# Optimization experiments

Hardware: AMD Instinct MI355X
Metric: run time of the kernel (lower is better)

The kernel has to match this reference:

```python
import jax, jax.numpy as jnp
import numpy as np

B, S, IN = 1, 50000, 128
N = B * S
E = 800000
HID, HEADS, OUT = 64, 2, 64
NEG_SLOPE = 0.2
BN_EPS = 1e-5


def setup_inputs() -> dict:
    key = jax.random.key(0)
    ks = jax.random.split(key, 12)
    s = 0.1
    return {
        "data": jax.random.normal(ks[0], (B, S, IN), jnp.float32),
        "edge_index": jax.random.randint(ks[1], (2, E), 0, N, dtype=jnp.int64),
        "W0": jax.random.normal(ks[2], (IN, HEADS * HID), jnp.float32) * s,
        "att_src0": jax.random.normal(ks[3], (HEADS, HID), jnp.float32) * s,
        "att_dst0": jax.random.normal(ks[4], (HEADS, HID), jnp.float32) * s,
        "bias0": jnp.zeros((HEADS * HID,), jnp.float32),
        "gamma0": jnp.ones((HEADS * HID,), jnp.float32),
        "beta0": jnp.zeros((HEADS * HID,), jnp.float32),
        "W1": jax.random.normal(ks[5], (HEADS * HID, OUT), jnp.float32) * s,
        "att_src1": jax.random.normal(ks[6], (1, OUT), jnp.float32) * s,
        "att_dst1": jax.random.normal(ks[7], (1, OUT), jnp.float32) * s,
        "bias1": jnp.zeros((OUT,), jnp.float32),
    }


def gat_conv(x, edge_index, W, att_src, att_dst, bias, heads, ch, concat):
    n = x.shape[0]
    loop = jnp.arange(n, dtype=edge_index.dtype)
    src = jnp.concatenate([edge_index[0], loop])  # PyG adds self-loops by default
    dst = jnp.concatenate([edge_index[1], loop])
    h = (x @ W).reshape(n, heads, ch)  # [N,H,C]
    a_src = (h * att_src).sum(-1)  # [N,H]
    a_dst = (h * att_dst).sum(-1)  # [N,H]
    e = jax.nn.leaky_relu(a_src[src] + a_dst[dst], NEG_SLOPE)  # [Etot,H]
    m = jax.ops.segment_max(e, dst, num_segments=n)  # segment softmax over dst
    ex = jnp.exp(e - m[dst])
    denom = jax.ops.segment_sum(ex, dst, num_segments=n)
    alpha = ex / (denom[dst] + 1e-16)  # [Etot,H]
    out = jax.ops.segment_sum(h[src] * alpha[:, :, None], dst, num_segments=n)  # [N,H,C]
    out = out.reshape(n, heads * ch) if concat else out.mean(axis=1)
    return out + bias


def reference(data, edge_index, W0, att_src0, att_dst0, bias0, gamma0, beta0,
              W1, att_src1, att_dst1, bias1):
    x = data.reshape(N, IN)
    x = gat_conv(x, edge_index, W0, att_src0, att_dst0, bias0, HEADS, HID, True)
    mu = x.mean(axis=0)
    var = x.var(axis=0)
    x = (x - mu) * jax.lax.rsqrt(var + BN_EPS) * gamma0 + beta0  # BatchNorm1d (batch stats)
    x = jax.nn.elu(x)
    x = gat_conv(x, edge_index, W1, att_src1, att_dst1, bias1, 1, OUT, False)
    return x.reshape(B, S, OUT)
```

## Files before the change

kernel.cpp:

```cpp
#include <hip/hip_runtime.h>
#include <hip/hip_fp16.h>
#include <math.h>

#define N_NODES 50000
#define E_EDGES 800000
#define NEG_SLOPE 0.2f
#define BN_EPS 1e-5f

#define BK_SHIFT 9
#define NBK 98
#define L1_BLOCKS 256
#define L1_CHUNK (E_EDGES / L1_BLOCKS)
#define CNT_N (NBK * L1_BLOCKS)
#define SCG_BLOCKS ((CNT_N + 1023) / 1024)
#define STAGE_MAX 9216

typedef __attribute__((ext_vector_type(8))) _Float16 half8;
typedef __attribute__((ext_vector_type(4))) float f32x4;

__device__ __forceinline__ float lrelu(float v) { return v > 0.f ? v : NEG_SLOPE * v; }

__global__ void k_zero(float* __restrict__ bn_sum, float* __restrict__ bn_sumsq) {
  int t = threadIdx.x;
  if (t < 128) { bn_sum[t] = 0.f; bn_sumsq[t] = 0.f; }
}

__global__ __launch_bounds__(256) void k_cvtx(const float* __restrict__ x,
                                              _Float16* __restrict__ xh) {
  int i = blockIdx.x * 256 + threadIdx.x;
  const float4* p = (const float4*)x + (size_t)i * 2;
  float4 a = p[0], b = p[1];
  half8 o = {(_Float16)a.x, (_Float16)a.y, (_Float16)a.z, (_Float16)a.w,
             (_Float16)b.x, (_Float16)b.y, (_Float16)b.z, (_Float16)b.w};
  *((half8*)xh + i) = o;
}

__global__ void k_cvtW(const float* __restrict__ W0, const float* __restrict__ W1,
                       _Float16* __restrict__ W0t, _Float16* __restrict__ W1t) {
  int t = threadIdx.x;
  for (int idx = t; idx < 128 * 128; idx += 256) {
    int k = idx >> 7, c = idx & 127;
    W0t[c * 128 + k] = (_Float16)W0[idx];
  }
  for (int idx = t; idx < 128 * 64; idx += 256) {
    int k = idx >> 6, c = idx & 63;
    W1t[c * 128 + k] = (_Float16)W1[idx];
  }
}

__global__ __launch_bounds__(256) void k_cvty(const float* __restrict__ x,
                                              const float* __restrict__ scale,
                                              const float* __restrict__ shift,
                                              _Float16* __restrict__ yh) {
  int i = blockIdx.x * 256 + threadIdx.x;
  int c = (i * 8) & 127;
  float4 s0 = *(const float4*)&scale[c], s1 = *(const float4*)&scale[c + 4];
  float4 f0 = *(const float4*)&shift[c], f1 = *(const float4*)&shift[c + 4];
  const float4* p = (const float4*)x + (size_t)i * 2;
  float4 a = p[0], b = p[1];
  float v[8];
  v[0] = a.x * s0.x + f0.x; v[1] = a.y * s0.y + f0.y;
  v[2] = a.z * s0.z + f0.z; v[3] = a.w * s0.w + f0.w;
  v[4] = b.x * s1.x + f1.x; v[5] = b.y * s1.y + f1.y;
  v[6] = b.z * s1.z + f1.z; v[7] = b.w * s1.w + f1.w;
  half8 o;
#pragma unroll
  for (int j = 0; j < 8; j++) {
    float e = v[j] > 0.f ? v[j] : __expf(v[j]) - 1.f;
    o[j] = (_Float16)e;
  }
  *((half8*)yh + i) = o;
}

__global__ __launch_bounds__(256) void k_l1hist(const int* __restrict__ dst,
                                                int* __restrict__ cnt) {
  __shared__ int lcnt[NBK];
  int t = threadIdx.x;
  if (t < NBK) lcnt[t] = 0;
  __syncthreads();
  int beg = blockIdx.x * L1_CHUNK, end = beg + L1_CHUNK;
  for (int e = beg + t; e < end; e += 256)
    atomicAdd(&lcnt[((unsigned int)dst[e]) >> BK_SHIFT], 1);
  __syncthreads();
  for (int b = t; b < NBK; b += 256) cnt[b * L1_BLOCKS + blockIdx.x] = lcnt[b];
}

__global__ __launch_bounds__(256) void k_scan1g(const int* __restrict__ cnt,
                                                int* __restrict__ tmp,
                                                int* __restrict__ bsums) {
  __shared__ int ts[256];
  int t = threadIdx.x;
  int base = blockIdx.x * 1024 + t * 4;
  int c0 = (base + 0 < CNT_N) ? cnt[base + 0] : 0;
  int c1 = (base + 1 < CNT_N) ? cnt[base + 1] : 0;
  int c2 = (base + 2 < CNT_N) ? cnt[base + 2] : 0;
  int c3 = (base + 3 < CNT_N) ? cnt[base + 3] : 0;
  int s = c0 + c1 + c2 + c3;
  ts[t] = s;
  __syncthreads();
  for (int off = 1; off < 256; off <<= 1) {
    int v = (t >= off) ? ts[t - off] : 0;
    __syncthreads();
    ts[t] += v;
    __syncthreads();
  }
  int excl = ts[t] - s;
  if (t == 255) bsums[blockIdx.x] = ts[255];
  if (base + 0 < CNT_N) tmp[base + 0] = excl;
  if (base + 1 < CNT_N) tmp[base + 1] = excl + c0;
  if (base + 2 < CNT_N) tmp[base + 2] = excl + c0 + c1;
  if (base + 3 < CNT_N) tmp[base + 3] = excl + c0 + c1 + c2;
}

__global__ void k_scan2g(int* __restrict__ bsums) {
  int t = threadIdx.x;
  int orig = (t < SCG_BLOCKS) ? bsums[t] : 0;
  int v = orig;
#pragma unroll
  for (int off = 1; off < 64; off <<= 1) {
    int u = __shfl_up(v, off);
    if (t >= off) v += u;
  }
  if (t < SCG_BLOCKS) bsums[t] = v - orig;
}

__global__ __launch_bounds__(256) void k_l1scatter(const int* __restrict__ src,
                                                   const int* __restrict__ dst,
                                                   const int* __restrict__ tmp,
                                                   const int* __restrict__ bsums,
                                                   unsigned int* __restrict__ binned) {
  __shared__ int cur[NBK];
  int t = threadIdx.x;
  for (int b = t; b < NBK; b += 256) {
    int idx = b * L1_BLOCKS + blockIdx.x;
    cur[b] = tmp[idx] + bsums[idx >> 10];
  }
  __syncthreads();
  int beg = blockIdx.x * L1_CHUNK, end = beg + L1_CHUNK;
  for (int e = beg + t; e < end; e += 256) {
    unsigned int d = (unsigned int)dst[e];
    int b = d >> BK_SHIFT;
    int p = atomicAdd(&cur[b], 1);
    binned[p] = ((unsigned int)src[e] << 16) | d;
  }
}

__global__ void k_bbase(const int* __restrict__ tmp, const int* __restrict__ bsums,
                        int* __restrict__ bucket_base) {
  int b = threadIdx.x;
  if (b < NBK) {
    int idx = b * L1_BLOCKS;
    bucket_base[b] = tmp[idx] + bsums[idx >> 10];
  }
  if (b == NBK) bucket_base[NBK] = E_EDGES;
}

__global__ __launch_bounds__(256) void k_scatter3(const int* __restrict__ bucket_base,
                                                  const unsigned int* __restrict__ binned,
                                                  int* __restrict__ row_ptr,
                                                  int* __restrict__ csr_src) {
  __shared__ int cnt[512];
  __shared__ int staging[STAGE_MAX];
  __shared__ int ts[256];
  int t = threadIdx.x;
  int b = blockIdx.x;
  int lo = b << BK_SHIFT;
  int hi = lo + 512; if (hi > N_NODES) hi = N_NODES;
  int nloc = hi - lo;
  int base = bucket_base[b];
  int end = bucket_base[b + 1];
  cnt[t] = 0; cnt[t + 256] = 0;
  __syncthreads();
  for (int i = base + t; i < end; i += 256)
    atomicAdd(&cnt[(binned[i] & 0xFFFFu) - lo], 1);
  __syncthreads();
  int c0 = cnt[2 * t], c1 = cnt[2 * t + 1];
  int pair = c0 + c1;
  ts[t] = pair;
  __syncthreads();
  for (int off = 1; off < 256; off <<= 1) {
    int v = (t >= off) ? ts[t - off] : 0;
    __syncthreads();
    ts[t] += v;
    __syncthreads();
  }
  int exclp = ts[t] - pair;
  cnt[2 * t] = exclp;
  cnt[2 * t + 1] = exclp + c0;
  if (2 * t < nloc) row_ptr[lo + 2 * t] = base + exclp;
  if (2 * t + 1 < nloc) row_ptr[lo + 2 * t + 1] = base + exclp + c0;
  if (b == NBK - 1 && t == 0) row_ptr[N_NODES] = E_EDGES;
  __syncthreads();
  for (int i = base + t; i < end; i += 256) {
    unsigned int v = binned[i];
    int d = (int)(v & 0xFFFFu) - lo;
    int p = atomicAdd(&cnt[d], 1);
    int s = (int)(v >> 16);
    if (p < STAGE_MAX) staging[p] = s;
    else csr_src[base + p] = s;
  }
  __syncthreads();
  int tot = end - base;
  int lim = tot < STAGE_MAX ? tot : STAGE_MAX;
  for (int k = t; k < lim; k += 256) csr_src[base + k] = staging[k];
}

__global__ __launch_bounds__(256) void k_gemm0m(
    const _Float16* __restrict__ xh, const _Float16* __restrict__ Wt,
    const float* __restrict__ att_s, const float* __restrict__ att_d,
    _Float16* __restrict__ h, float* __restrict__ a_src, float* __restrict__ a_dst) {
  int lane = threadIdx.x & 63;
  int wv = threadIdx.x >> 6;
  int row0 = blockIdx.x * 64 + wv * 16;
  int m = lane & 15, kg = lane >> 4;
  int arow = row0 + m;
  int arowc = arow < N_NODES ? arow : N_NODES - 1;
  f32x4 acc[8];
#pragma unroll
  for (int ct = 0; ct < 8; ct++) acc[ct] = (f32x4){0.f, 0.f, 0.f, 0.f};
#pragma unroll
  for (int kc = 0; kc < 4; kc++) {
    half8 af = *(const half8*)&xh[(size_t)arowc * 128 + kc * 32 + kg * 8];
#pragma unroll
    for (int ct = 0; ct < 8; ct++) {
      half8 bf = *(const half8*)&Wt[(ct * 16 + m) * 128 + kc * 32 + kg * 8];
      acc[ct] = __builtin_amdgcn_mfma_f32_16x16x32_f16(af, bf, acc[ct], 0, 0, 0);
    }
  }
  float as[8], ad[8];
#pragma unroll
  for (int ct = 0; ct < 8; ct++) { as[ct] = att_s[ct * 16 + m]; ad[ct] = att_d[ct * 16 + m]; }
#pragma unroll
  for (int r = 0; r < 4; r++) {
    int row = row0 + kg * 4 + r;
    bool ok = row < N_NODES;
    float ps0 = 0.f, pd0 = 0.f, ps1 = 0.f, pd1 = 0.f;
#pragma unroll
    for (int ct = 0; ct < 4; ct++) { ps0 += acc[ct][r] * as[ct]; pd0 += acc[ct][r] * ad[ct]; }
#pragma unroll
    for (int ct = 4; ct < 8; ct++) { ps1 += acc[ct][r] * as[ct]; pd1 += acc[ct][r] * ad[ct]; }
#pragma unroll
    for (int msk = 1; msk <= 8; msk <<= 1) {
      ps0 += __shfl_xor(ps0, msk); pd0 += __shfl_xor(pd0, msk);
      ps1 += __shfl_xor(ps1, msk); pd1 += __shfl_xor(pd1, msk);
    }
    if (ok) {
#pragma unroll
      for (int ct = 0; ct < 8; ct++)
        h[(size_t)row * 128 + ct * 16 + m] = (_Float16)acc[ct][r];
      if (m == 0) {
        a_src[row * 2 + 0] = ps0; a_dst[row * 2 + 0] = pd0;
        a_src[row * 2 + 1] = ps1; a_dst[row * 2 + 1] = pd1;
      }
    }
  }
}

__global__ __launch_bounds__(256) void k_gemm1m(
    const _Float16* __restrict__ yh, const _Float16* __restrict__ Wt,
    const float* __restrict__ att_s, const float* __restrict__ att_d,
    _Float16* __restrict__ h, float* __restrict__ a_src, float* __restrict__ a_dst) {
  int lane = threadIdx.x & 63;
  int wv = threadIdx.x >> 6;
  int row0 = blockIdx.x * 64 + wv * 16;
  int m = lane & 15, kg = lane >> 4;
  int arow = row0 + m;
  int arowc = arow < N_NODES ? arow : N_NODES - 1;
  f32x4 acc[4];
#pragma unroll
  for (int ct = 0; ct < 4; ct++) acc[ct] = (f32x4){0.f, 0.f, 0.f, 0.f};
#pragma unroll
  for (int kc = 0; kc < 4; kc++) {
    half8 af = *(const half8*)&yh[(size_t)arowc * 128 + kc * 32 + kg * 8];
#pragma unroll
    for (int ct = 0; ct < 4; ct++) {
      half8 bf = *(const half8*)&Wt[(ct * 16 + m) * 128 + kc * 32 + kg * 8];
      acc[ct] = __builtin_amdgcn_mfma_f32_16x16x32_f16(af, bf, acc[ct], 0, 0, 0);
    }
  }
  float as[4], ad[4];
#pragma unroll
  for (int ct = 0; ct < 4; ct++) { as[ct] = att_s[ct * 16 + m]; ad[ct] = att_d[ct * 16 + m]; }
#pragma unroll
  for (int r = 0; r < 4; r++) {
    int row = row0 + kg * 4 + r;
    bool ok = row < N_NODES;
    float ps = 0.f, pd = 0.f;
#pragma unroll
    for (int ct = 0; ct < 4; ct++) { ps += acc[ct][r] * as[ct]; pd += acc[ct][r] * ad[ct]; }
#pragma unroll
    for (int msk = 1; msk <= 8; msk <<= 1) {
      ps += __shfl_xor(ps, msk); pd += __shfl_xor(pd, msk);
    }
    if (ok) {
#pragma unroll
      for (int ct = 0; ct < 4; ct++)
        h[(size_t)row * 64 + ct * 16 + m] = (_Float16)acc[ct][r];
      if (m == 0) { a_src[row] = ps; a_dst[row] = pd; }
    }
  }
}

__global__ __launch_bounds__(256) void k_agg0(
    const int* __restrict__ row_ptr, const int* __restrict__ csr_src,
    const __half* __restrict__ h, const float* __restrict__ a_src,
    const float* __restrict__ a_dst, const float* __restrict__ bias,
    float* __restrict__ out) {
  int node = (blockIdx.x * blockDim.x + threadIdx.x) >> 6;
  if (node >= N_NODES) return;
  int l = threadIdx.x & 63;
  int head = l >> 5;
  int c = l * 2;
  float ad = a_dst[node * 2 + head];
  float m = lrelu(a_src[node * 2 + head] + ad);
  float d = 1.f;
  float2 hv = __half22float2(*(const __half2*)&h[(size_t)node * 128 + c]);
  float acc0 = hv.x, acc1 = hv.y;
  int beg = row_ptr[node], end = row_ptr[node + 1];
  int i = beg;
  for (; i + 8 <= end; i += 8) {
    int s0 = csr_src[i], s1 = csr_src[i + 1], s2 = csr_src[i + 2], s3 = csr_src[i + 3];
    int s4 = csr_src[i + 4], s5 = csr_src[i + 5], s6 = csr_src[i + 6], s7 = csr_src[i + 7];
    float e0 = lrelu(a_src[s0 * 2 + head] + ad), e1 = lrelu(a_src[s1 * 2 + head] + ad);
    float e2 = lrelu(a_src[s2 * 2 + head] + ad), e3 = lrelu(a_src[s3 * 2 + head] + ad);
    float e4 = lrelu(a_src[s4 * 2 + head] + ad), e5 = lrelu(a_src[s5 * 2 + head] + ad);
    float e6 = lrelu(a_src[s6 * 2 + head] + ad), e7 = lrelu(a_src[s7 * 2 + head] + ad);
    __half2 p0 = *(const __half2*)&h[(size_t)s0 * 128 + c];
    __half2 p1 = *(const __half2*)&h[(size_t)s1 * 128 + c];
    __half2 p2 = *(const __half2*)&h[(size_t)s2 * 128 + c];
    __half2 p3 = *(const __half2*)&h[(size_t)s3 * 128 + c];
    __half2 p4 = *(const __half2*)&h[(size_t)s4 * 128 + c];
    __half2 p5 = *(const __half2*)&h[(size_t)s5 * 128 + c];
    __half2 p6 = *(const __half2*)&h[(size_t)s6 * 128 + c];
    __half2 p7 = *(const __half2*)&h[(size_t)s7 * 128 + c];
    float nm = fmaxf(m, fmaxf(fmaxf(fmaxf(e0, e1), fmaxf(e2, e3)),
                              fmaxf(fmaxf(e4, e5), fmaxf(e6, e7))));
    float sc = __expf(m - nm);
    float w0 = __expf(e0 - nm), w1 = __expf(e1 - nm), w2 = __expf(e2 - nm), w3 = __expf(e3 - nm);
    float w4 = __expf(e4 - nm), w5 = __expf(e5 - nm), w6 = __expf(e6 - nm), w7 = __expf(e7 - nm);
    d = d * sc + ((w0 + w1) + (w2 + w3)) + ((w4 + w5) + (w6 + w7));
    float2 f0 = __half22float2(p0), f1 = __half22float2(p1);
    float2 f2 = __half22float2(p2), f3 = __half22float2(p3);
    float2 f4 = __half22float2(p4), f5 = __half22float2(p5);
    float2 f6 = __half22float2(p6), f7 = __half22float2(p7);
    acc0 = acc0 * sc + (w0 * f0.x + w1 * f1.x + w2 * f2.x + w3 * f3.x) +
           (w4 * f4.x + w5 * f5.x + w6 * f6.x + w7 * f7.x);
    acc1 = acc1 * sc + (w0 * f0.y + w1 * f1.y + w2 * f2.y + w3 * f3.y) +
           (w4 * f4.y + w5 * f5.y + w6 * f6.y + w7 * f7.y);
    m = nm;
  }
  for (; i + 4 <= end; i += 4) {
    int s0 = csr_src[i], s1 = csr_src[i + 1], s2 = csr_src[i + 2], s3 = csr_src[i + 3];
    float e0 = lrelu(a_src[s0 * 2 + head] + ad), e1 = lrelu(a_src[s1 * 2 + head] + ad);
    float e2 = lrelu(a_src[s2 * 2 + head] + ad), e3 = lrelu(a_src[s3 * 2 + head] + ad);
    __half2 p0 = *(const __half2*)&h[(size_t)s0 * 128 + c];
    __half2 p1 = *(const __half2*)&h[(size_t)s1 * 128 + c];
    __half2 p2 = *(const __half2*)&h[(size_t)s2 * 128 + c];
    __half2 p3 = *(const __half2*)&h[(size_t)s3 * 128 + c];
    float nm = fmaxf(fmaxf(m, e0), fmaxf(fmaxf(e1, e2), e3));
    float sc = __expf(m - nm);
    float w0 = __expf(e0 - nm), w1 = __expf(e1 - nm), w2 = __expf(e2 - nm), w3 = __expf(e3 - nm);
    d = d * sc + (w0 + w1) + (w2 + w3);
    float2 f0 = __half22float2(p0), f1 = __half22float2(p1);
    float2 f2 = __half22float2(p2), f3 = __half22float2(p3);
    acc0 = acc0 * sc + w0 * f0.x + w1 * f1.x + w2 * f2.x + w3 * f3.x;
    acc1 = acc1 * sc + w0 * f0.y + w1 * f1.y + w2 * f2.y + w3 * f3.y;
    m = nm;
  }
  for (; i < end; i++) {
    int s = csr_src[i];
    float ee = lrelu(a_src[s * 2 + head] + ad);
    __half2 pp = *(const __half2*)&h[(size_t)s * 128 + c];
    float nm = fmaxf(m, ee);
    float sc = __expf(m - nm);
    float w = __expf(ee - nm);
    float2 ff = __half22float2(pp);
    d = d * sc + w;
    acc0 = acc0 * sc + w * ff.x;
    acc1 = acc1 * sc + w * ff.y;
    m = nm;
  }
  float inv = 1.f / d;
  float2 o;
  o.x = acc0 * inv + bias[c];
  o.y = acc1 * inv + bias[c + 1];
  *(float2*)&out[(size_t)node * 128 + c] = o;
}

__global__ __launch_bounds__(256) void k_bnstats(const float* __restrict__ x,
                                                 float* __restrict__ bn_sum,
                                                 float* __restrict__ bn_sumsq) {
  int f = threadIdx.x & 127;
  int half = threadIdx.x >> 7;
  float s = 0.f, s2 = 0.f;
  for (int r = blockIdx.x * 2 + half; r < N_NODES; r += gridDim.x * 2) {
    float v = x[(size_t)r * 128 + f];
    s += v;
    s2 += v * v;
  }
  __shared__ float ls[256], ls2[256];
  ls[threadIdx.x] = s;
  ls2[threadIdx.x] = s2;
  __syncthreads();
  if (half == 0) {
    atomicAdd(&bn_sum[f], s + ls[f + 128]);
    atomicAdd(&bn_sumsq[f], s2 + ls2[f + 128]);
  }
}

__global__ void k_bnfinal(const float* __restrict__ sum, const float* __restrict__ sumsq,
                          const float* __restrict__ gamma, const float* __restrict__ beta,
                          float* __restrict__ scale, float* __restrict__ shift) {
  int f = threadIdx.x;
  float mu = sum[f] / (float)N_NODES;
  float var = sumsq[f] / (float)N_NODES - mu * mu;
  float sc = gamma[f] * rsqrtf(var + BN_EPS);
  scale[f] = sc;
  shift[f] = beta[f] - mu * sc;
}

__global__ __launch_bounds__(256) void k_agg1(
    const int* __restrict__ row_ptr, const int* __restrict__ csr_src,
    const __half* __restrict__ h, const float* __restrict__ a_src,
    const float* __restrict__ a_dst, const float* __restrict__ bias,
    float* __restrict__ out) {
  int node = (blockIdx.x * blockDim.x + threadIdx.x) >> 6;
  if (node >= N_NODES) return;
  int l = threadIdx.x & 63;
  float ad = a_dst[node];
  float m = lrelu(a_src[node] + ad);
  float d = 1.f;
  float acc = __half2float(h[(size_t)node * 64 + l]);
  int beg = row_ptr[node], end = row_ptr[node + 1];
  int i = beg;
  for (; i + 8 <= end; i += 8) {
    int s0 = csr_src[i], s1 = csr_src[i + 1], s2 = csr_src[i + 2], s3 = csr_src[i + 3];
    int s4 = csr_src[i + 4], s5 = csr_src[i + 5], s6 = csr_src[i + 6], s7 = csr_src[i + 7];
    float e0 = lrelu(a_src[s0] + ad), e1 = lrelu(a_src[s1] + ad);
    float e2 = lrelu(a_src[s2] + ad), e3 = lrelu(a_src[s3] + ad);
    float e4 = lrelu(a_src[s4] + ad), e5 = lrelu(a_src[s5] + ad);
    float e6 = lrelu(a_src[s6] + ad), e7 = lrelu(a_src[s7] + ad);
    __half p0 = h[(size_t)s0 * 64 + l], p1 = h[(size_t)s1 * 64 + l];
    __half p2 = h[(size_t)s2 * 64 + l], p3 = h[(size_t)s3 * 64 + l];
    __half p4 = h[(size_t)s4 * 64 + l], p5 = h[(size_t)s5 * 64 + l];
    __half p6 = h[(size_t)s6 * 64 + l], p7 = h[(size_t)s7 * 64 + l];
    float nm = fmaxf(m, fmaxf(fmaxf(fmaxf(e0, e1), fmaxf(e2, e3)),
                              fmaxf(fmaxf(e4, e5), fmaxf(e6, e7))));
    float sc = __expf(m - nm);
    float w0 = __expf(e0 - nm), w1 = __expf(e1 - nm), w2 = __expf(e2 - nm), w3 = __expf(e3 - nm);
    float w4 = __expf(e4 - nm), w5 = __expf(e5 - nm), w6 = __expf(e6 - nm), w7 = __expf(e7 - nm);
    d = d * sc + ((w0 + w1) + (w2 + w3)) + ((w4 + w5) + (w6 + w7));
    acc = acc * sc +
          (w0 * __half2float(p0) + w1 * __half2float(p1) + w2 * __half2float(p2) +
           w3 * __half2float(p3)) +
          (w4 * __half2float(p4) + w5 * __half2float(p5) + w6 * __half2float(p6) +
           w7 * __half2float(p7));
    m = nm;
  }
  for (; i + 4 <= end; i += 4) {
    int s0 = csr_src[i], s1 = csr_src[i + 1], s2 = csr_src[i + 2], s3 = csr_src[i + 3];
    float e0 = lrelu(a_src[s0] + ad), e1 = lrelu(a_src[s1] + ad);
    float e2 = lrelu(a_src[s2] + ad), e3 = lrelu(a_src[s3] + ad);
    __half p0 = h[(size_t)s0 * 64 + l], p1 = h[(size_t)s1 * 64 + l];
    __half p2 = h[(size_t)s2 * 64 + l], p3 = h[(size_t)s3 * 64 + l];
    float nm = fmaxf(fmaxf(m, e0), fmaxf(fmaxf(e1, e2), e3));
    float sc = __expf(m - nm);
    float w0 = __expf(e0 - nm), w1 = __expf(e1 - nm), w2 = __expf(e2 - nm), w3 = __expf(e3 - nm);
    d = d * sc + (w0 + w1) + (w2 + w3);
    acc = acc * sc + w0 * __half2float(p0) + w1 * __half2float(p1) + w2 * __half2float(p2) +
          w3 * __half2float(p3);
    m = nm;
  }
  for (; i < end; i++) {
    int s = csr_src[i];
    float ee = lrelu(a_src[s] + ad);
    __half pp = h[(size_t)s * 64 + l];
    float nm = fmaxf(m, ee);
    float sc = __expf(m - nm);
    float w = __expf(ee - nm);
    d = d * sc + w;
    acc = acc * sc + w * __half2float(pp);
    m = nm;
  }
  out[(size_t)node * 64 + l] = acc / d + bias[l];
}

extern "C" void kernel_launch(void* const* d_in, const int* in_sizes, int n_in,
                              void* d_out, int out_size, void* d_ws, size_t ws_size,
                              hipStream_t stream) {
  const float* data = (const float*)d_in[0];
  const int* ei = (const int*)d_in[1];
  const float* W0 = (const float*)d_in[2];
  const float* att_src0 = (const float*)d_in[3];
  const float* att_dst0 = (const float*)d_in[4];
  const float* bias0 = (const float*)d_in[5];
  const float* gamma0 = (const float*)d_in[6];
  const float* beta0 = (const float*)d_in[7];
  const float* W1 = (const float*)d_in[8];
  const float* att_src1 = (const float*)d_in[9];
  const float* att_dst1 = (const float*)d_in[10];
  const float* bias1 = (const float*)d_in[11];
  float* out = (float*)d_out;

  char* ws = (char*)d_ws;
  size_t off = 0;
  auto alloc = [&](size_t bytes) -> void* {
    void* p = ws + off;
    off = (off + bytes + 255) & ~(size_t)255;
    return p;
  };
  int* cnt = (int*)alloc((size_t)CNT_N * 4);
  int* tmp = (int*)alloc((size_t)CNT_N * 4);
  int* bsums = (int*)alloc(32 * 4);
  int* bucket_base = (int*)alloc((NBK + 1) * 4);
  int* row_ptr = (int*)alloc((N_NODES + 1) * 4);
  unsigned int* binned = (unsigned int*)alloc((size_t)E_EDGES * 4);
  int* csr_src = (int*)alloc((size_t)E_EDGES * 4);
  _Float16* xh = (_Float16*)alloc((size_t)N_NODES * 128 * 2);
  _Float16* W0t = (_Float16*)alloc(128 * 128 * 2);
  _Float16* W1t = (_Float16*)alloc(64 * 128 * 2);
  _Float16* h0 = (_Float16*)alloc((size_t)N_NODES * 128 * 2);
  float* a_s0 = (float*)alloc((size_t)N_NODES * 2 * 4);
  float* a_d0 = (float*)alloc((size_t)N_NODES * 2 * 4);
  float* out0 = (float*)alloc((size_t)N_NODES * 128 * 4);
  _Float16* yh = (_Float16*)alloc((size_t)N_NODES * 128 * 2);
  float* bn_sum = (float*)alloc(128 * 4);
  float* bn_sumsq = (float*)alloc(128 * 4);
  float* bn_scale = (float*)alloc(128 * 4);
  float* bn_shift = (float*)alloc(128 * 4);
  _Float16* h1 = h0;
  float* a_s1 = a_s0;
  float* a_d1 = a_d0;

  const int* srcArr = ei;
  const int* dstArr = ei + E_EDGES;

  k_zero<<<1, 128, 0, stream>>>(bn_sum, bn_sumsq);
  k_cvtW<<<1, 256, 0, stream>>>(W0, W1, W0t, W1t);
  k_cvtx<<<3125, 256, 0, stream>>>(data, xh);
  k_l1hist<<<L1_BLOCKS, 256, 0, stream>>>(dstArr, cnt);
  k_scan1g<<<SCG_BLOCKS, 256, 0, stream>>>(cnt, tmp, bsums);
  k_scan2g<<<1, 64, 0, stream>>>(bsums);
  k_l1scatter<<<L1_BLOCKS, 256, 0, stream>>>(srcArr, dstArr, tmp, bsums, binned);
  k_bbase<<<1, 128, 0, stream>>>(tmp, bsums, bucket_base);
  k_scatter3<<<NBK, 256, 0, stream>>>(bucket_base, binned, row_ptr, csr_src);
  k_gemm0m<<<(N_NODES + 63) / 64, 256, 0, stream>>>(xh, W0t, att_src0, att_dst0, h0, a_s0, a_d0);
  k_agg0<<<(N_NODES + 3) / 4, 256, 0, stream>>>(row_ptr, csr_src, (const __half*)h0, a_s0, a_d0,
                                                bias0, out0);
  k_bnstats<<<1024, 256, 0, stream>>>(out0, bn_sum, bn_sumsq);
  k_bnfinal<<<1, 128, 0, stream>>>(bn_sum, bn_sumsq, gamma0, beta0, bn_scale, bn_shift);
  k_cvty<<<3125, 256, 0, stream>>>(out0, bn_scale, bn_shift, yh);
  k_gemm1m<<<(N_NODES + 63) / 64, 256, 0, stream>>>(yh, W1t, att_src1, att_dst1, h1, a_s1, a_d1);
  k_agg1<<<(N_NODES + 3) / 4, 256, 0, stream>>>(row_ptr, csr_src, (const __half*)h1, a_s1, a_d1,
                                                bias1, out);
}
```

Baseline: 307.5 us.

## Fuse input conversions into GEMMs and split aggregation into weight and accumulate passes

The fp32-to-fp16 conversion of the input and the BatchNorm+ELU conversion are folded into the GEMM A-operand loads, which removes two elementwise kernels and their fp16 intermediate buffers. Each GAT aggregation is split in two. A wave-parallel kernel computes the normalized softmax weights per edge and writes them to memory. A second kernel gathers features using those precomputed weights, with no online max/rescale in the inner loop. This adds an extra pass over the CSR and an edge-weight array to write and read back, in exchange for a simpler, more parallel accumulate loop.

```diff
diff --git a/kernel.cpp b/kernel.cpp
--- a/kernel.cpp
+++ b/kernel.cpp
@@ -25,16 +25,6 @@
   if (t < 128) { bn_sum[t] = 0.f; bn_sumsq[t] = 0.f; }
 }
 
-__global__ __launch_bounds__(256) void k_cvtx(const float* __restrict__ x,
-                                              _Float16* __restrict__ xh) {
-  int i = blockIdx.x * 256 + threadIdx.x;
-  const float4* p = (const float4*)x + (size_t)i * 2;
-  float4 a = p[0], b = p[1];
-  half8 o = {(_Float16)a.x, (_Float16)a.y, (_Float16)a.z, (_Float16)a.w,
-             (_Float16)b.x, (_Float16)b.y, (_Float16)b.z, (_Float16)b.w};
-  *((half8*)xh + i) = o;
-}
-
 __global__ void k_cvtW(const float* __restrict__ W0, const float* __restrict__ W1,
                        _Float16* __restrict__ W0t, _Float16* __restrict__ W1t) {
   int t = threadIdx.x;
@@ -46,30 +36,6 @@
     int k = idx >> 6, c = idx & 63;
     W1t[c * 128 + k] = (_Float16)W1[idx];
   }
-}
-
-__global__ __launch_bounds__(256) void k_cvty(const float* __restrict__ x,
-                                              const float* __restrict__ scale,
-                                              const float* __restrict__ shift,
-                                              _Float16* __restrict__ yh) {
-  int i = blockIdx.x * 256 + threadIdx.x;
-  int c = (i * 8) & 127;
-  float4 s0 = *(const float4*)&scale[c], s1 = *(const float4*)&scale[c + 4];
-  float4 f0 = *(const float4*)&shift[c], f1 = *(const float4*)&shift[c + 4];
-  const float4* p = (const float4*)x + (size_t)i * 2;
-  float4 a = p[0], b = p[1];
-  float v[8];
-  v[0] = a.x * s0.x + f0.x; v[1] = a.y * s0.y + f0.y;
-  v[2] = a.z * s0.z + f0.z; v[3] = a.w * s0.w + f0.w;
-  v[4] = b.x * s1.x + f1.x; v[5] = b.y * s1.y + f1.y;
-  v[6] = b.z * s1.z + f1.z; v[7] = b.w * s1.w + f1.w;
-  half8 o;
-#pragma unroll
-  for (int j = 0; j < 8; j++) {
-    float e = v[j] > 0.f ? v[j] : __expf(v[j]) - 1.f;
-    o[j] = (_Float16)e;
-  }
-  *((half8*)yh + i) = o;
 }
 
 __global__ __launch_bounds__(256) void k_l1hist(const int* __restrict__ dst,
@@ -206,7 +172,7 @@
 }
 
 __global__ __launch_bounds__(256) void k_gemm0m(
-    const _Float16* __restrict__ xh, const _Float16* __restrict__ Wt,
+    const float* __restrict__ x, const _Float16* __restrict__ Wt,
     const float* __restrict__ att_s, const float* __restrict__ att_d,
     _Float16* __restrict__ h, float* __restrict__ a_src, float* __restrict__ a_dst) {
   int lane = threadIdx.x & 63;
@@ -220,7 +186,11 @@
   for (int ct = 0; ct < 8; ct++) acc[ct] = (f32x4){0.f, 0.f, 0.f, 0.f};
 #pragma unroll
   for (int kc = 0; kc < 4; kc++) {
-    half8 af = *(const half8*)&xh[(size_t)arowc * 128 + kc * 32 + kg * 8];
+    const float* xp = &x[(size_t)arowc * 128 + kc * 32 + kg * 8];
+    float4 xa = *(const float4*)xp;
+    float4 xb = *(const float4*)(xp + 4);
+    half8 af = {(_Float16)xa.x, (_Float16)xa.y, (_Float16)xa.z, (_Float16)xa.w,
+                (_Float16)xb.x, (_Float16)xb.y, (_Float16)xb.z, (_Float16)xb.w};
 #pragma unroll
     for (int ct = 0; ct < 8; ct++) {
       half8 bf = *(const half8*)&Wt[(ct * 16 + m) * 128 + kc * 32 + kg * 8];
@@ -257,7 +227,8 @@
 }
 
 __global__ __launch_bounds__(256) void k_gemm1m(
-    const _Float16* __restrict__ yh, const _Float16* __restrict__ Wt,
+    const float* __restrict__ y, const float* __restrict__ scale,
+    const float* __restrict__ shift, const _Float16* __restrict__ Wt,
     const float* __restrict__ att_s, const float* __restrict__ att_d,
     _Float16* __restrict__ h, float* __restrict__ a_src, float* __restrict__ a_dst) {
   int lane = threadIdx.x & 63;
@@ -271,10 +242,26 @@
   for (int ct = 0; ct < 4; ct++) acc[ct] = (f32x4){0.f, 0.f, 0.f, 0.f};
 #pragma unroll
   for (int kc = 0; kc < 4; kc++) {
-    half8 af = *(const half8*)&yh[(size_t)arowc * 128 + kc * 32 + kg * 8];
+    int kb = kc * 32 + kg * 8;
+    const float* yp = &y[(size_t)arowc * 128 + kb];
+    float4 ya = *(const float4*)yp;
+    float4 yb = *(const float4*)(yp + 4);
+    float4 sa = *(const float4*)&scale[kb], sb = *(const float4*)&scale[kb + 4];
+    float4 fa = *(const float4*)&shift[kb], fb = *(const float4*)&shift[kb + 4];
+    float v[8];
+    v[0] = ya.x * sa.x + fa.x; v[1] = ya.y * sa.y + fa.y;
+    v[2] = ya.z * sa.z + fa.z; v[3] = ya.w * sa.w + fa.w;
+    v[4] = yb.x * sb.x + fb.x; v[5] = yb.y * sb.y + fb.y;
+    v[6] = yb.z * sb.z + fb.z; v[7] = yb.w * sb.w + fb.w;
+    half8 af;
+#pragma unroll
+    for (int j = 0; j < 8; j++) {
+      float e = v[j] > 0.f ? v[j] : __expf(v[j]) - 1.f;
+      af[j] = (_Float16)e;
+    }
 #pragma unroll
     for (int ct = 0; ct < 4; ct++) {
-      half8 bf = *(const half8*)&Wt[(ct * 16 + m) * 128 + kc * 32 + kg * 8];
+      half8 bf = *(const half8*)&Wt[(ct * 16 + m) * 128 + kb];
       acc[ct] = __builtin_amdgcn_mfma_f32_16x16x32_f16(af, bf, acc[ct], 0, 0, 0);
     }
   }
@@ -301,89 +288,93 @@
   }
 }
 
-__global__ __launch_bounds__(256) void k_agg0(
+__global__ __launch_bounds__(256) void k_wts0(
     const int* __restrict__ row_ptr, const int* __restrict__ csr_src,
-    const __half* __restrict__ h, const float* __restrict__ a_src,
-    const float* __restrict__ a_dst, const float* __restrict__ bias,
+    const float* __restrict__ a_src, const float* __restrict__ a_dst,
+    float2* __restrict__ wts, float2* __restrict__ selfw) {
+  int node = (blockIdx.x * blockDim.x + threadIdx.x) >> 6;
+  if (node >= N_NODES) return;
+  int l = threadIdx.x & 63;
+  float ad0 = a_dst[node * 2], ad1 = a_dst[node * 2 + 1];
+  float es0 = lrelu(a_src[node * 2] + ad0);
+  float es1 = lrelu(a_src[node * 2 + 1] + ad1);
+  int beg = row_ptr[node], end = row_ptr[node + 1];
+  const float NEGBIG = -3.0e38f;
+  float m0 = NEGBIG, s0 = 0.f, m1 = NEGBIG, s1 = 0.f;
+  for (int j = beg + l; j < end; j += 64) {
+    int s = csr_src[j];
+    float e0 = lrelu(a_src[s * 2] + ad0);
+    float e1 = lrelu(a_src[s * 2 + 1] + ad1);
+    float nm0 = fmaxf(m0, e0);
+    s0 = s0 * __expf(m0 - nm0) + __expf(e0 - nm0); m0 = nm0;
+    float nm1 = fmaxf(m1, e1);
+    s1 = s1 * __expf(m1 - nm1) + __expf(e1 - nm1); m1 = nm1;
+  }
+#pragma unroll
+  for (int msk = 1; msk < 64; msk <<= 1) {
+    float om0 = __shfl_xor(m0, msk), os0 = __shfl_xor(s0, msk);
+    float nm0 = fmaxf(m0, om0);
+    s0 = s0 * __expf(m0 - nm0) + os0 * __expf(om0 - nm0); m0 = nm0;
+    float om1 = __shfl_xor(m1, msk), os1 = __shfl_xor(s1, msk);
+    float nm1 = fmaxf(m1, om1);
+    s1 = s1 * __expf(m1 - nm1) + os1 * __expf(om1 - nm1); m1 = nm1;
+  }
+  float fm0 = fmaxf(m0, es0);
+  float d0 = s0 * __expf(m0 - fm0) + __expf(es0 - fm0);
+  float fm1 = fmaxf(m1, es1);
+  float d1 = s1 * __expf(m1 - fm1) + __expf(es1 - fm1);
+  float inv0 = 1.f / d0, inv1 = 1.f / d1;
+  for (int j = beg + l; j < end; j += 64) {
+    int s = csr_src[j];
+    float e0 = lrelu(a_src[s * 2] + ad0);
+    float e1 = lrelu(a_src[s * 2 + 1] + ad1);
+    wts[j] = make_float2(__expf(e0 - fm0) * inv0, __expf(e1 - fm1) * inv1);
+  }
+  if (l == 0) selfw[node] = make_float2(__expf(es0 - fm0) * inv0, __expf(es1 - fm1) * inv1);
+}
+
+__global__ __launch_bounds__(256) void k_acc0(
+    const int* __restrict__ row_ptr, const int* __restrict__ csr_src,
+    const __half* __restrict__ h, const float2* __restrict__ wts,
+    const float2* __restrict__ selfw, const float* __restrict__ bias,
     float* __restrict__ out) {
   int node = (blockIdx.x * blockDim.x + threadIdx.x) >> 6;
   if (node >= N_NODES) return;
   int l = threadIdx.x & 63;
   int head = l >> 5;
   int c = l * 2;
-  float ad = a_dst[node * 2 + head];
-  float m = lrelu(a_src[node * 2 + head] + ad);
-  float d = 1.f;
+  float2 sw = selfw[node];
+  float aself = head ? sw.y : sw.x;
   float2 hv = __half22float2(*(const __half2*)&h[(size_t)node * 128 + c]);
-  float acc0 = hv.x, acc1 = hv.y;
+  float acc0 = aself * hv.x, acc1 = aself * hv.y;
+  float bcc0 = 0.f, bcc1 = 0.f;
   int beg = row_ptr[node], end = row_ptr[node + 1];
-  int i = beg;
-  for (; i + 8 <= end; i += 8) {
-    int s0 = csr_src[i], s1 = csr_src[i + 1], s2 = csr_src[i + 2], s3 = csr_src[i + 3];
-    int s4 = csr_src[i + 4], s5 = csr_src[i + 5], s6 = csr_src[i + 6], s7 = csr_src[i + 7];
-    float e0 = lrelu(a_src[s0 * 2 + head] + ad), e1 = lrelu(a_src[s1 * 2 + head] + ad);
-    float e2 = lrelu(a_src[s2 * 2 + head] + ad), e3 = lrelu(a_src[s3 * 2 + head] + ad);
-    float e4 = lrelu(a_src[s4 * 2 + head] + ad), e5 = lrelu(a_src[s5 * 2 + head] + ad);
-    float e6 = lrelu(a_src[s6 * 2 + head] + ad), e7 = lrelu(a_src[s7 * 2 + head] + ad);
-    __half2 p0 = *(const __half2*)&h[(size_t)s0 * 128 + c];
-    __half2 p1 = *(const __half2*)&h[(size_t)s1 * 128 + c];
-    __half2 p2 = *(const __half2*)&h[(size_t)s2 * 128 + c];
-    __half2 p3 = *(const __half2*)&h[(size_t)s3 * 128 + c];
-    __half2 p4 = *(const __half2*)&h[(size_t)s4 * 128 + c];
-    __half2 p5 = *(const __half2*)&h[(size_t)s5 * 128 + c];
-    __half2 p6 = *(const __half2*)&h[(size_t)s6 * 128 + c];
-    __half2 p7 = *(const __half2*)&h[(size_t)s7 * 128 + c];
-    float nm = fmaxf(m, fmaxf(fmaxf(fmaxf(e0, e1), fmaxf(e2, e3)),
-                              fmaxf(fmaxf(e4, e5), fmaxf(e6, e7))));
-    float sc = __expf(m - nm);
-    float w0 = __expf(e0 - nm), w1 = __expf(e1 - nm), w2 = __expf(e2 - nm), w3 = __expf(e3 - nm);
-    float w4 = __expf(e4 - nm), w5 = __expf(e5 - nm), w6 = __expf(e6 - nm), w7 = __expf(e7 - nm);
-    d = d * sc + ((w0 + w1) + (w2 + w3)) + ((w4 + w5) + (w6 + w7));
-    float2 f0 = __half22float2(p0), f1 = __half22float2(p1);
-    float2 f2 = __half22float2(p2), f3 = __half22float2(p3);
-    float2 f4 = __half22float2(p4), f5 = __half22float2(p5);
-    float2 f6 = __half22float2(p6), f7 = __half22float2(p7);
-    acc0 = acc0 * sc + (w0 * f0.x + w1 * f1.x + w2 * f2.x + w3 * f3.x) +
-           (w4 * f4.x + w5 * f5.x + w6 * f6.x + w7 * f7.x);
-    acc1 = acc1 * sc + (w0 * f0.y + w1 * f1.y + w2 * f2.y + w3 * f3.y) +
-           (w4 * f4.y + w5 * f5.y + w6 * f6.y + w7 * f7.y);
-    m = nm;
-  }
-  for (; i + 4 <= end; i += 4) {
-    int s0 = csr_src[i], s1 = csr_src[i + 1], s2 = csr_src[i + 2], s3 = csr_src[i + 3];
-    float e0 = lrelu(a_src[s0 * 2 + head] + ad), e1 = lrelu(a_src[s1 * 2 + head] + ad);
-    float e2 = lrelu(a_src[s2 * 2 + head] + ad), e3 = lrelu(a_src[s3 * 2 + head] + ad);
-    __half2 p0 = *(const __half2*)&h[(size_t)s0 * 128 + c];
-    __half2 p1 = *(const __half2*)&h[(size_t)s1 * 128 + c];
-    __half2 p2 = *(const __half2*)&h[(size_t)s2 * 128 + c];
-    __half2 p3 = *(const __half2*)&h[(size_t)s3 * 128 + c];
-    float nm = fmaxf(fmaxf(m, e0), fmaxf(fmaxf(e1, e2), e3));
-    float sc = __expf(m - nm);
-    float w0 = __expf(e0 - nm), w1 = __expf(e1 - nm), w2 = __expf(e2 - nm), w3 = __expf(e3 - nm);
-    d = d * sc + (w0 + w1) + (w2 + w3);
-    float2 f0 = __half22float2(p0), f1 = __half22float2(p1);
-    float2 f2 = __half22float2(p2), f3 = __half22float2(p3);
-    acc0 = acc0 * sc + w0 * f0.x + w1 * f1.x + w2 * f2.x + w3 * f3.x;
-    acc1 = acc1 * sc + w0 * f0.y + w1 * f1.y + w2 * f2.y + w3 * f3.y;
-    m = nm;
-  }
-  for (; i < end; i++) {
-    int s = csr_src[i];
-    float ee = lrelu(a_src[s * 2 + head] + ad);
-    __half2 pp = *(const __half2*)&h[(size_t)s * 128 + c];
-    float nm = fmaxf(m, ee);
-    float sc = __expf(m - nm);
-    float w = __expf(ee - nm);
-    float2 ff = __half22float2(pp);
-    d = d * sc + w;
-    acc0 = acc0 * sc + w * ff.x;
-    acc1 = acc1 * sc + w * ff.y;
-    m = nm;
-  }
-  float inv = 1.f / d;
+  int j = beg;
+  for (; j + 4 <= end; j += 4) {
+    int s0 = csr_src[j], s1 = csr_src[j + 1], s2 = csr_src[j + 2], s3 = csr_src[j + 3];
+    float2 w0 = wts[j], w1 = wts[j + 1], w2 = wts[j + 2], w3 = wts[j + 3];
+    float a0 = head ? w0.y : w0.x, a1 = head ? w1.y : w1.x;
+    float a2 = head ? w2.y : w2.x, a3 = head ? w3.y : w3.x;
+    float2 f0 = __half22float2(*(const __half2*)&h[(size_t)s0 * 128 + c]);
+    float2 f1 = __half22float2(*(const __half2*)&h[(size_t)s1 * 128 + c]);
+    float2 f2 = __half22float2(*(const __half2*)&h[(size_t)s2 * 128 + c]);
+    float2 f3 = __half22float2(*(const __half2*)&h[(size_t)s3 * 128 + c]);
+    acc0 += a0 * f0.x + a2 * f2.x;
+    bcc0 += a1 * f1.x + a3 * f3.x;
+    acc1 += a0 * f0.y + a2 * f2.y;
+    bcc1 += a1 * f1.y + a3 * f3.y;
+  }
+  for (; j < end; j++) {
+    int s = csr_src[j];
+    float2 w = wts[j];
+    float a = head ? w.y : w.x;
+    float2 f = __half22float2(*(const __half2*)&h[(size_t)s * 128 + c]);
+    acc0 += a * f.x;
+    acc1 += a * f.y;
+  }
   float2 o;
-  o.x = acc0 * inv + bias[c];
-  o.y = acc1 * inv + bias[c + 1];
+  o.x = acc0 + bcc0 + bias[c];
+  o.y = acc1 + bcc1 + bias[c + 1];
   *(float2*)&out[(size_t)node * 128 + c] = o;
 }
 
@@ -419,70 +410,68 @@
   shift[f] = beta[f] - mu * sc;
 }
 
-__global__ __launch_bounds__(256) void k_agg1(
+__global__ __launch_bounds__(256) void k_wts1(
     const int* __restrict__ row_ptr, const int* __restrict__ csr_src,
-    const __half* __restrict__ h, const float* __restrict__ a_src,
-    const float* __restrict__ a_dst, const float* __restrict__ bias,
+    const float* __restrict__ a_src, const float* __restrict__ a_dst,
+    float* __restrict__ wts, float* __restrict__ selfw) {
+  int node = (blockIdx.x * blockDim.x + threadIdx.x) >> 6;
+  if (node >= N_NODES) return;
+  int l = threadIdx.x & 63;
+  float ad = a_dst[node];
+  float es = lrelu(a_src[node] + ad);
+  int beg = row_ptr[node], end = row_ptr[node + 1];
+  const float NEGBIG = -3.0e38f;
+  float m = NEGBIG, s = 0.f;
+  for (int j = beg + l; j < end; j += 64) {
+    int sn = csr_src[j];
+    float e = lrelu(a_src[sn] + ad);
+    float nm = fmaxf(m, e);
+    s = s * __expf(m - nm) + __expf(e - nm); m = nm;
+  }
+#pragma unroll
+  for (int msk = 1; msk < 64; msk <<= 1) {
+    float om = __shfl_xor(m, msk), os = __shfl_xor(s, msk);
+    float nm = fmaxf(m, om);
+    s = s * __expf(m - nm) + os * __expf(om - nm); m = nm;
+  }
+  float fm = fmaxf(m, es);
+  float d = s * __expf(m - fm) + __expf(es - fm);
+  float inv = 1.f / d;
+  for (int j = beg + l; j < end; j += 64) {
+    int sn = csr_src[j];
+    float e = lrelu(a_src[sn] + ad);
+    wts[j] = __expf(e - fm) * inv;
+  }
+  if (l == 0) selfw[node] = __expf(es - fm) * inv;
+}
+
+__global__ __launch_bounds__(256) void k_acc1(
+    const int* __restrict__ row_ptr, const int* __restrict__ csr_src,
+    const __half* __restrict__ h, const float* __restrict__ wts,
+    const float* __restrict__ selfw, const float* __restrict__ bias,
     float* __restrict__ out) {
   int node = (blockIdx.x * blockDim.x + threadIdx.x) >> 6;
   if (node >= N_NODES) return;
   int l = threadIdx.x & 63;
-  float ad = a_dst[node];
-  float m = lrelu(a_src[node] + ad);
-  float d = 1.f;
-  float acc = __half2float(h[(size_t)node * 64 + l]);
+  float acc = selfw[node] * __half2float(h[(size_t)node * 64 + l]);
+  float bcc = 0.f;
   int beg = row_ptr[node], end = row_ptr[node + 1];
-  int i = beg;
-  for (; i + 8 <= end; i += 8) {
-    int s0 = csr_src[i], s1 = csr_src[i + 1], s2 = csr_src[i + 2], s3 = csr_src[i + 3];
-    int s4 = csr_src[i + 4], s5 = csr_src[i + 5], s6 = csr_src[i + 6], s7 = csr_src[i + 7];
-    float e0 = lrelu(a_src[s0] + ad), e1 = lrelu(a_src[s1] + ad);
-    float e2 = lrelu(a_src[s2] + ad), e3 = lrelu(a_src[s3] + ad);
-    float e4 = lrelu(a_src[s4] + ad), e5 = lrelu(a_src[s5] + ad);
-    float e6 = lrelu(a_src[s6] + ad), e7 = lrelu(a_src[s7] + ad);
-    __half p0 = h[(size_t)s0 * 64 + l], p1 = h[(size_t)s1 * 64 + l];
-    __half p2 = h[(size_t)s2 * 64 + l], p3 = h[(size_t)s3 * 64 + l];
-    __half p4 = h[(size_t)s4 * 64 + l], p5 = h[(size_t)s5 * 64 + l];
-    __half p6 = h[(size_t)s6 * 64 + l], p7 = h[(size_t)s7 * 64 + l];
-    float nm = fmaxf(m, fmaxf(fmaxf(fmaxf(e0, e1), fmaxf(e2, e3)),
-                              fmaxf(fmaxf(e4, e5), fmaxf(e6, e7))));
-    float sc = __expf(m - nm);
-    float w0 = __expf(e0 - nm), w1 = __expf(e1 - nm), w2 = __expf(e2 - nm), w3 = __expf(e3 - nm);
-    float w4 = __expf(e4 - nm), w5 = __expf(e5 - nm), w6 = __expf(e6 - nm), w7 = __expf(e7 - nm);
-    d = d * sc + ((w0 + w1) + (w2 + w3)) + ((w4 + w5) + (w6 + w7));
-    acc = acc * sc +
-          (w0 * __half2float(p0) + w1 * __half2float(p1) + w2 * __half2float(p2) +
-           w3 * __half2float(p3)) +
-          (w4 * __half2float(p4) + w5 * __half2float(p5) + w6 * __half2float(p6) +
-           w7 * __half2float(p7));
-    m = nm;
-  }
-  for (; i + 4 <= end; i += 4) {
-    int s0 = csr_src[i], s1 = csr_src[i + 1], s2 = csr_src[i + 2], s3 = csr_src[i + 3];
-    float e0 = lrelu(a_src[s0] + ad), e1 = lrelu(a_src[s1] + ad);
-    float e2 = lrelu(a_src[s2] + ad), e3 = lrelu(a_src[s3] + ad);
-    __half p0 = h[(size_t)s0 * 64 + l], p1 = h[(size_t)s1 * 64 + l];
-    __half p2 = h[(size_t)s2 * 64 + l], p3 = h[(size_t)s3 * 64 + l];
-    float nm = fmaxf(fmaxf(m, e0), fmaxf(fmaxf(e1, e2), e3));
-    float sc = __expf(m - nm);
-    float w0 = __expf(e0 - nm), w1 = __expf(e1 - nm), w2 = __expf(e2 - nm), w3 = __expf(e3 - nm);
-    d = d * sc + (w0 + w1) + (w2 + w3);
-    acc = acc * sc + w0 * __half2float(p0) + w1 * __half2float(p1) + w2 * __half2float(p2) +
-          w3 * __half2float(p3);
-    m = nm;
-  }
-  for (; i < end; i++) {
-    int s = csr_src[i];
-    float ee = lrelu(a_src[s] + ad);
-    __half pp = h[(size_t)s * 64 + l];
-    float nm = fmaxf(m, ee);
-    float sc = __expf(m - nm);
-    float w = __expf(ee - nm);
-    d = d * sc + w;
-    acc = acc * sc + w * __half2float(pp);
-    m = nm;
-  }
-  out[(size_t)node * 64 + l] = acc / d + bias[l];
+  int j = beg;
+  for (; j + 4 <= end; j += 4) {
+    int s0 = csr_src[j], s1 = csr_src[j + 1], s2 = csr_src[j + 2], s3 = csr_src[j + 3];
+    float a0 = wts[j], a1 = wts[j + 1], a2 = wts[j + 2], a3 = wts[j + 3];
+    float f0 = __half2float(h[(size_t)s0 * 64 + l]);
+    float f1 = __half2float(h[(size_t)s1 * 64 + l]);
+    float f2 = __half2float(h[(size_t)s2 * 64 + l]);
+    float f3 = __half2float(h[(size_t)s3 * 64 + l]);
+    acc += a0 * f0 + a2 * f2;
+    bcc += a1 * f1 + a3 * f3;
+  }
+  for (; j < end; j++) {
+    int s = csr_src[j];
+    acc += wts[j] * __half2float(h[(size_t)s * 64 + l]);
+  }
+  out[(size_t)node * 64 + l] = acc + bcc + bias[l];
 }
 
 extern "C" void kernel_launch(void* const* d_in, const int* in_sizes, int n_in,
@@ -516,14 +505,14 @@
   int* row_ptr = (int*)alloc((N_NODES + 1) * 4);
   unsigned int* binned = (unsigned int*)alloc((size_t)E_EDGES * 4);
   int* csr_src = (int*)alloc((size_t)E_EDGES * 4);
-  _Float16* xh = (_Float16*)alloc((size_t)N_NODES * 128 * 2);
   _Float16* W0t = (_Float16*)alloc(128 * 128 * 2);
   _Float16* W1t = (_Float16*)alloc(64 * 128 * 2);
   _Float16* h0 = (_Float16*)alloc((size_t)N_NODES * 128 * 2);
   float* a_s0 = (float*)alloc((size_t)N_NODES * 2 * 4);
   float* a_d0 = (float*)alloc((size_t)N_NODES * 2 * 4);
+  float2* wts0 = (float2*)alloc((size_t)E_EDGES * 8);
+  float2* selfw0 = (float2*)alloc((size_t)N_NODES * 8);
   float* out0 = (float*)alloc((size_t)N_NODES * 128 * 4);
-  _Float16* yh = (_Float16*)alloc((size_t)N_NODES * 128 * 2);
   float* bn_sum = (float*)alloc(128 * 4);
   float* bn_sumsq = (float*)alloc(128 * 4);
   float* bn_scale = (float*)alloc(128 * 4);
@@ -531,26 +520,30 @@
   _Float16* h1 = h0;
   float* a_s1 = a_s0;
   float* a_d1 = a_d0;
+  float* wts1 = (float*)wts0;
+  float* selfw1 = (float*)selfw0;
 
   const int* srcArr = ei;
   const int* dstArr = ei + E_EDGES;
 
   k_zero<<<1, 128, 0, stream>>>(bn_sum, bn_sumsq);
   k_cvtW<<<1, 256, 0, stream>>>(W0, W1, W0t, W1t);
-  k_cvtx<<<3125, 256, 0, stream>>>(data, xh);
   k_l1hist<<<L1_BLOCKS, 256, 0, stream>>>(dstArr, cnt);
   k_scan1g<<<SCG_BLOCKS, 256, 0, stream>>>(cnt, tmp, bsums);
   k_scan2g<<<1, 64, 0, stream>>>(bsums);
   k_l1scatter<<<L1_BLOCKS, 256, 0, stream>>>(srcArr, dstArr, tmp, bsums, binned);
   k_bbase<<<1, 128, 0, stream>>>(tmp, bsums, bucket_base);
   k_scatter3<<<NBK, 256, 0, stream>>>(bucket_base, binned, row_ptr, csr_src);
-  k_gemm0m<<<(N_NODES + 63) / 64, 256, 0, stream>>>(xh, W0t, att_src0, att_dst0, h0, a_s0, a_d0);
-  k_agg0<<<(N_NODES + 3) / 4, 256, 0, stream>>>(row_ptr, csr_src, (const __half*)h0, a_s0, a_d0,
-                                                bias0, out0);
+  k_gemm0m<<<(N_NODES + 63) / 64, 256, 0, stream>>>(data, W0t, att_src0, att_dst0, h0, a_s0,
+                                                    a_d0);
+  k_wts0<<<(N_NODES + 3) / 4, 256, 0, stream>>>(row_ptr, csr_src, a_s0, a_d0, wts0, selfw0);
+  k_acc0<<<(N_NODES + 3) / 4, 256, 0, stream>>>(row_ptr, csr_src, (const __half*)h0, wts0,
+                                                selfw0, bias0, out0);
   k_bnstats<<<1024, 256, 0, stream>>>(out0, bn_sum, bn_sumsq);
   k_bnfinal<<<1, 128, 0, stream>>>(bn_sum, bn_sumsq, gamma0, beta0, bn_scale, bn_shift);
-  k_cvty<<<3125, 256, 0, stream>>>(out0, bn_scale, bn_shift, yh);
-  k_gemm1m<<<(N_NODES + 63) / 64, 256, 0, stream>>>(yh, W1t, att_src1, att_dst1, h1, a_s1, a_d1);
-  k_agg1<<<(N_NODES + 3) / 4, 256, 0, stream>>>(row_ptr, csr_src, (const __half*)h1, a_s1, a_d1,
-                                                bias1, out);
-}
+  k_gemm1m<<<(N_NODES + 63) / 64, 256, 0, stream>>>(out0, bn_scale, bn_shift, W1t, att_src1,
+                                                    att_dst1, h1, a_s1, a_d1);
+  k_wts1<<<(N_NODES + 3) / 4, 256, 0, stream>>>(row_ptr, csr_src, a_s1, a_d1, wts1, selfw1);
+  k_acc1<<<(N_NODES + 3) / 4, 256, 0, stream>>>(row_ptr, csr_src, (const __half*)h1, wts1,
+                                                selfw1, bias1, out);
+}
```

Result: slower. 345.4 us (+12.3%).
